# Performance work log

Measured on AMD Instinct MI355X. Metric: run time of the kernel, lower is better.

The kernel has to match this reference:

```python
import jax, jax.numpy as jnp
import numpy as np

N_NODES = 50000
N_EDGES = 600000
DIM = 128
N_LAYERS = 3
N_GRAPHS = 512
BN_EPS = 1e-5


def setup_inputs() -> dict:
    key = jax.random.key(0)
    ks = jax.random.split(key, 8)
    x = jax.random.normal(ks[0], (N_NODES, DIM), dtype=jnp.float32)
    edge_index = jax.random.randint(ks[1], (2, N_EDGES), 0, N_NODES, dtype=jnp.int32)
    batch = jnp.sort(jax.random.randint(ks[2], (N_NODES,), 0, N_GRAPHS, dtype=jnp.int32))
    W1s = jax.random.normal(ks[3], (N_LAYERS, DIM, DIM), dtype=jnp.float32) * (1.0 / np.sqrt(DIM))
    b1s = jnp.zeros((N_LAYERS, DIM), dtype=jnp.float32)
    W2s = jax.random.normal(ks[4], (N_LAYERS, DIM, DIM), dtype=jnp.float32) * (1.0 / np.sqrt(DIM))
    b2s = jnp.zeros((N_LAYERS, DIM), dtype=jnp.float32)
    gammas = jnp.ones((N_LAYERS, DIM), dtype=jnp.float32)
    betas = jnp.zeros((N_LAYERS, DIM), dtype=jnp.float32)
    return {"x": x, "edge_index": edge_index, "batch": batch,
            "W1s": W1s, "b1s": b1s, "W2s": W2s, "b2s": b2s,
            "gammas": gammas, "betas": betas}


def reference(x, edge_index, batch, W1s, b1s, W2s, b2s, gammas, betas):
    # EncoderGIN.forward: stack of GINConv (eps=0) -> ReLU -> BatchNorm1d (train mode),
    # then global_add_pool per layer and concat along feature dim.
    n_nodes = x.shape[0]
    src, dst = edge_index[0], edge_index[1]
    h = x
    pools = []
    for i in range(N_LAYERS):
        # GINConv: aggregate sum of neighbor feats at dst, add (1+0)*self
        agg = jax.ops.segment_sum(h[src], dst, num_segments=n_nodes) + h
        # MLP: Linear -> ReLU -> Linear
        h1 = jax.nn.relu(agg @ W1s[i] + b1s[i])
        h2 = h1 @ W2s[i] + b2s[i]
        # outer ReLU
        h2 = jax.nn.relu(h2)
        # BatchNorm1d, training mode (biased variance over the node dim)
        mean = jnp.mean(h2, axis=0)
        var = jnp.var(h2, axis=0)
        h = (h2 - mean) * jax.lax.rsqrt(var + BN_EPS) * gammas[i] + betas[i]
        pools.append(jax.ops.segment_sum(h, batch, num_segments=N_GRAPHS))
    return jnp.concatenate(pools, axis=1)  # [N_GRAPHS, N_LAYERS*DIM]
```

## Files before the change

### kernel.cpp

```cpp
#include <hip/hip_runtime.h>

#define N_NODES 50000
#define N_EDGES 600000
#define DIM 128
#define N_GRAPHS 512
#define N_LAYERS 3
#define OUT_STRIDE (N_LAYERS * DIM)
#define BN_EPS 1e-5f
#define N_REP 16
#define CAP 64

#define NPB 128
#define NBIN 391
#define BCAP_BIN 3072
#define PADC 16
#define EPB 4096
#define NB3 147

#define NTILES 1563
#define NPAD (NTILES * 32)
#define AGG_BLOCKS 2048

typedef __attribute__((ext_vector_type(8))) short short8;
typedef __attribute__((ext_vector_type(4))) float floatx4;

__device__ inline short f2bf(float f) {
    union { float f; unsigned u; } x{f};
    unsigned r = x.u + 0x7fffu + ((x.u >> 16) & 1u);
    return (short)(r >> 16);
}
__device__ inline float bf2f(short h) {
    union { unsigned u; float f; } x;
    x.u = ((unsigned)(unsigned short)h) << 16;
    return x.f;
}
__device__ inline void split_trunc(float f, short& hi, short& lo) {
    union { float f; unsigned u; } x{f};
    hi = (short)(x.u >> 16);
    union { unsigned u; float f; } hf;
    hf.u = x.u & 0xffff0000u;
    union { float f; unsigned u; } y{f - hf.f};
    lo = (short)(y.u >> 16);
}
__device__ inline floatx4 bf4_to_f4(uint2 w) {
    union { unsigned u; float f; } a, b, c, d;
    a.u = w.x << 16;
    b.u = w.x & 0xffff0000u;
    c.u = w.y << 16;
    d.u = w.y & 0xffff0000u;
    return floatx4{a.f, b.f, c.f, d.f};
}

__global__ __launch_bounds__(256) void prep_scatter_kernel(const int* __restrict__ src,
                                                           const int* __restrict__ dst,
                                                           int* __restrict__ binCur,
                                                           int2* __restrict__ binned,
                                                           const float* __restrict__ W1s,
                                                           const float* __restrict__ W2s,
                                                           short* __restrict__ Whi,
                                                           short* __restrict__ Wlo,
                                                           const float* __restrict__ x,
                                                           short* __restrict__ xb,
                                                           short* __restrict__ hbA,
                                                           short* __restrict__ hbB) {
    if (blockIdx.x < NB3) {
        __shared__ int hist[NBIN];
        __shared__ int basev[NBIN];
        const int t = threadIdx.x;
        for (int b = t; b < NBIN; b += 256) hist[b] = 0;
        __syncthreads();
        const int e0 = blockIdx.x * EPB;
        int sreg[16], dreg[16], rreg[16];
#pragma unroll
        for (int k = 0; k < 16; ++k) {
            int e = e0 + k * 256 + t;
            if (e < N_EDGES) {
                sreg[k] = src[e];
                dreg[k] = dst[e];
            } else {
                dreg[k] = -1;
            }
        }
#pragma unroll
        for (int k = 0; k < 16; ++k)
            if (dreg[k] >= 0) rreg[k] = atomicAdd(&hist[dreg[k] >> 7], 1);
        __syncthreads();
        for (int b = t; b < NBIN; b += 256) {
            int c = hist[b];
            basev[b] = (c > 0) ? atomicAdd(&binCur[b * PADC], c) : 0;
        }
        __syncthreads();
#pragma unroll
        for (int k = 0; k < 16; ++k)
            if (dreg[k] >= 0) {
                int b = dreg[k] >> 7;
                int pos = basev[b] + rreg[k];
                if (pos < BCAP_BIN)
                    binned[(size_t)b * BCAP_BIN + pos] = make_int2(sreg[k], dreg[k] & (NPB - 1));
            }
        return;
    }
    int i = (blockIdx.x - NB3) * 256 + threadIdx.x;
    if (i < 6 * DIM * DIM) {
        int mat = i >> 14;
        int e = i & 16383;
        int k = e >> 7, n = e & 127;
        const float* W = (mat < 3) ? (W1s + (size_t)mat * DIM * DIM)
                                   : (W2s + (size_t)(mat - 3) * DIM * DIM);
        float w = W[e];
        short hi = f2bf(w);
        short lo = f2bf(w - bf2f(hi));
        size_t o = ((size_t)mat << 14) + n * DIM + k;
        Whi[o] = hi;
        Wlo[o] = lo;
    }
    if (i < N_NODES * 32) {
        float4 v = ((const float4*)x)[i];
        unsigned lo = (unsigned short)f2bf(v.x) | ((unsigned)(unsigned short)f2bf(v.y) << 16);
        unsigned hi = (unsigned short)f2bf(v.z) | ((unsigned)(unsigned short)f2bf(v.w) << 16);
        ((uint2*)xb)[i] = make_uint2(lo, hi);
    } else if (i < (N_NODES + 1) * 32) {
        ((uint2*)xb)[i] = make_uint2(0u, 0u);
        ((uint2*)hbA)[i] = make_uint2(0u, 0u);
        ((uint2*)hbB)[i] = make_uint2(0u, 0u);
    }
}

__global__ __launch_bounds__(256) void bucket_build_kernel(const int* __restrict__ binCur,
                                                           const int2* __restrict__ binned,
                                                           int* __restrict__ deg,
                                                           int* __restrict__ esrc) {
    __shared__ int ldeg[NPB];
    __shared__ int lbuck[NPB * CAP];
    const int b = blockIdx.x;
    const int t = threadIdx.x;
    for (int i = t; i < NPB * CAP; i += 256) lbuck[i] = N_NODES;
    if (t < NPB) ldeg[t] = 0;
    __syncthreads();
    int n = binCur[b * PADC];
    if (n > BCAP_BIN) n = BCAP_BIN;
    const int2* bp = binned + (size_t)b * BCAP_BIN;
    for (int i = t; i < n; i += 256) {
        int2 e = bp[i];
        int slot = atomicAdd(&ldeg[e.y], 1);
        if (slot < CAP) lbuck[(e.y << 6) + slot] = e.x;
    }
    __syncthreads();
    const int node0 = b * NPB;
    const int nvalid = min(NPB, N_NODES - node0);
    if (t < NPB && t < nvalid) deg[node0 + t] = ldeg[t];
    const int nu4 = nvalid << 4;
    uint4* d4 = (uint4*)(esrc + ((size_t)node0 << 6));
    const uint4* s4 = (const uint4*)lbuck;
    for (int i = t; i < nu4; i += 256) d4[i] = s4[i];
}

__global__ __launch_bounds__(256) void agg_kernel(const short* __restrict__ hin,
                                                  const int* __restrict__ deg,
                                                  const int* __restrict__ esrc,
                                                  const float* __restrict__ prevrep,
                                                  const float* __restrict__ pgamma,
                                                  const float* __restrict__ pbeta,
                                                  unsigned* __restrict__ agg) {
    __shared__ float GO_s[256];
    const int tid = threadIdx.x;
    if (prevrep) {
        float s = 0.f;
#pragma unroll
        for (int r = 0; r < N_REP; ++r) s += prevrep[r * 256 + tid];
        GO_s[tid] = s;
        __syncthreads();
        if (tid < 128) {
            const float invn = 1.0f / (float)N_NODES;
            float m = GO_s[tid] * invn;
            float var = GO_s[128 + tid] * invn - m * m;
            float G = pgamma[tid] * rsqrtf(var + BN_EPS);
            GO_s[tid] = G;
            GO_s[128 + tid] = pbeta[tid] - m * G;
        }
    } else {
        GO_s[tid] = (tid < 128) ? 1.f : 0.f;
    }
    __syncthreads();

    const int hw = tid >> 5;
    const int l32 = tid & 31;
    floatx4 G4 = *(const floatx4*)&GO_s[4 * l32];
    floatx4 O4 = *(const floatx4*)&GO_s[128 + 4 * l32];
    const uint2* hb = (const uint2*)hin;

    for (int node = blockIdx.x * 8 + hw; node < NPAD; node += AGG_BLOCKS * 8) {
        floatx4 acc = {0.f, 0.f, 0.f, 0.f};
        if (node < N_NODES) {
            int dgr = deg[node];
            if (dgr > CAP) dgr = CAP;
            const uint4* ep = (const uint4*)(esrc + ((size_t)node << 6));
            uint4 q0 = ep[0], q1 = ep[1], q2 = ep[2], q3 = ep[3];
            uint2 wself = hb[(size_t)node * 32 + l32];
            uint2 wv[16];
            wv[0] = hb[(size_t)q0.x * 32 + l32];
            wv[1] = hb[(size_t)q0.y * 32 + l32];
            wv[2] = hb[(size_t)q0.z * 32 + l32];
            wv[3] = hb[(size_t)q0.w * 32 + l32];
            wv[4] = hb[(size_t)q1.x * 32 + l32];
            wv[5] = hb[(size_t)q1.y * 32 + l32];
            wv[6] = hb[(size_t)q1.z * 32 + l32];
            wv[7] = hb[(size_t)q1.w * 32 + l32];
            wv[8] = hb[(size_t)q2.x * 32 + l32];
            wv[9] = hb[(size_t)q2.y * 32 + l32];
            wv[10] = hb[(size_t)q2.z * 32 + l32];
            wv[11] = hb[(size_t)q2.w * 32 + l32];
            wv[12] = hb[(size_t)q3.x * 32 + l32];
            wv[13] = hb[(size_t)q3.y * 32 + l32];
            wv[14] = hb[(size_t)q3.z * 32 + l32];
            wv[15] = hb[(size_t)q3.w * 32 + l32];
            floatx4 t0 = (bf4_to_f4(wv[0]) + bf4_to_f4(wv[1])) + (bf4_to_f4(wv[2]) + bf4_to_f4(wv[3]));
            floatx4 t1 = (bf4_to_f4(wv[4]) + bf4_to_f4(wv[5])) + (bf4_to_f4(wv[6]) + bf4_to_f4(wv[7]));
            floatx4 t2 = (bf4_to_f4(wv[8]) + bf4_to_f4(wv[9])) + (bf4_to_f4(wv[10]) + bf4_to_f4(wv[11]));
            floatx4 t3 = (bf4_to_f4(wv[12]) + bf4_to_f4(wv[13])) + (bf4_to_f4(wv[14]) + bf4_to_f4(wv[15]));
            acc = bf4_to_f4(wself) + ((t0 + t1) + (t2 + t3));
            if (dgr > 16) {
                int b0 = node << 6;
                int jend = b0 + ((dgr + 7) & ~7);
                for (int j = b0 + 16; j < jend; j += 8) {
                    uint4 i0 = *(const uint4*)&esrc[j];
                    uint4 i1 = *(const uint4*)&esrc[j + 4];
                    uint2 w0 = hb[(size_t)i0.x * 32 + l32];
                    uint2 w1 = hb[(size_t)i0.y * 32 + l32];
                    uint2 w2 = hb[(size_t)i0.z * 32 + l32];
                    uint2 w3 = hb[(size_t)i0.w * 32 + l32];
                    uint2 w4 = hb[(size_t)i1.x * 32 + l32];
                    uint2 w5 = hb[(size_t)i1.y * 32 + l32];
                    uint2 w6 = hb[(size_t)i1.z * 32 + l32];
                    uint2 w7 = hb[(size_t)i1.w * 32 + l32];
                    acc += ((bf4_to_f4(w0) + bf4_to_f4(w1)) + (bf4_to_f4(w2) + bf4_to_f4(w3))) +
                           ((bf4_to_f4(w4) + bf4_to_f4(w5)) + (bf4_to_f4(w6) + bf4_to_f4(w7)));
                }
            }
            float dp1 = (float)(dgr + 1);
            acc = G4 * acc + dp1 * O4;
        }
        short hi[4], lo[4];
#pragma unroll
        for (int q = 0; q < 4; ++q) split_trunc(acc[q], hi[q], lo[q]);
        unsigned p0 = ((unsigned)(unsigned short)hi[0] << 16) | (unsigned short)lo[0];
        unsigned p1 = ((unsigned)(unsigned short)hi[1] << 16) | (unsigned short)lo[1];
        unsigned p2 = ((unsigned)(unsigned short)hi[2] << 16) | (unsigned short)lo[2];
        unsigned p3 = ((unsigned)(unsigned short)hi[3] << 16) | (unsigned short)lo[3];
        *(uint4*)&agg[(size_t)node * 128 + 4 * l32] = make_uint4(p0, p1, p2, p3);
    }
}

__global__ __launch_bounds__(256, 6) void mlp_kernel(
    const unsigned* __restrict__ agg,
    const short* __restrict__ W1hi, const short* __restrict__ W1lo,
    const float* __restrict__ b1,
    const short* __restrict__ W2hi, const short* __restrict__ W2lo,
    const float* __restrict__ b2,
    const int* __restrict__ batch,
    short* __restrict__ out,
    float* __restrict__ srep,
    float* __restrict__ gout,
    int layer) {
    __shared__ unsigned sbuf[4096];
    const int tid = threadIdx.x;
    const int base = blockIdx.x * 32;

    {
        const uint4* gs = (const uint4*)(agg + (size_t)base * 128);
#pragma unroll
        for (int k = 0; k < 4; ++k) {
            uint4 v = gs[k * 256 + tid];
            int idx = (k * 256 + tid) * 4;
            int row = idx >> 7, c0 = idx & 127;
            *(uint4*)&sbuf[row * 128 + (((c0 >> 2) ^ (row & 31)) << 2)] = v;
        }
    }
    __syncthreads();

    const int wave = tid >> 6;
    const int lane = tid & 63;
    const int l15 = lane & 15;
    const int quad = lane >> 4;

    floatx4 acc[2][2];
#pragma unroll
    for (int mi = 0; mi < 2; ++mi)
#pragma unroll
        for (int nl = 0; nl < 2; ++nl) acc[mi][nl] = floatx4{0.f, 0.f, 0.f, 0.f};
#pragma unroll
    for (int ks = 0; ks < 4; ++ks) {
        short8 ahi[2], alo[2], bhi[2], blo[2];
#pragma unroll
        for (int mi = 0; mi < 2; ++mi) {
            int row = mi * 16 + l15;
            int c5 = ks * 8 + quad * 2;
            unsigned w[8];
            *(uint4*)&w[0] = *(const uint4*)&sbuf[row * 128 + ((c5 ^ (row & 31)) * 4)];
            *(uint4*)&w[4] = *(const uint4*)&sbuf[row * 128 + (((c5 + 1) ^ (row & 31)) * 4)];
#pragma unroll
            for (int j = 0; j < 8; ++j) {
                ahi[mi][j] = (short)(w[j] >> 16);
                alo[mi][j] = (short)(w[j] & 0xffffu);
            }
        }
#pragma unroll
        for (int nl = 0; nl < 2; ++nl) {
            size_t p = (size_t)((wave * 2 + nl) * 16 + l15) * DIM + ks * 32 + quad * 8;
            bhi[nl] = *(const short8*)&W1hi[p];
            blo[nl] = *(const short8*)&W1lo[p];
        }
#pragma unroll
        for (int mi = 0; mi < 2; ++mi)
#pragma unroll
            for (int nl = 0; nl < 2; ++nl) {
                acc[mi][nl] = __builtin_amdgcn_mfma_f32_16x16x32_bf16(ahi[mi], bhi[nl], acc[mi][nl], 0, 0, 0);
                acc[mi][nl] = __builtin_amdgcn_mfma_f32_16x16x32_bf16(alo[mi], bhi[nl], acc[mi][nl], 0, 0, 0);
                acc[mi][nl] = __builtin_amdgcn_mfma_f32_16x16x32_bf16(ahi[mi], blo[nl], acc[mi][nl], 0, 0, 0);
            }
    }
    __syncthreads();

#pragma unroll
    for (int mi = 0; mi < 2; ++mi)
#pragma unroll
        for (int nl = 0; nl < 2; ++nl) {
            int col = (wave * 2 + nl) * 16 + l15;
            float bv = b1[col];
#pragma unroll
            for (int reg = 0; reg < 4; ++reg) {
                int row = mi * 16 + quad * 4 + reg;
                float v = fmaxf(acc[mi][nl][reg] + bv, 0.f);
                union { float f; unsigned u; } x{v};
                union { unsigned u; float f; } hf;
                hf.u = x.u & 0xffff0000u;
                union { float f; unsigned u; } y{v - hf.f};
                unsigned w = hf.u | (y.u >> 16);
                sbuf[row * 128 + ((((col >> 2) ^ (row & 31)) * 4) + (col & 3))] = w;
            }
        }
    __syncthreads();

    floatx4 acc2[2][2];
#pragma unroll
    for (int mi = 0; mi < 2; ++mi)
#pragma unroll
        for (int nl = 0; nl < 2; ++nl) acc2[mi][nl] = floatx4{0.f, 0.f, 0.f, 0.f};
#pragma unroll
    for (int ks = 0; ks < 4; ++ks) {
        short8 ahi2[2], alo2[2], bhi[2], blo[2];
#pragma unroll
        for (int mi = 0; mi < 2; ++mi) {
            int row = mi * 16 + l15;
            int c5 = ks * 8 + quad * 2;
            unsigned w[8];
            *(uint4*)&w[0] = *(const uint4*)&sbuf[row * 128 + ((c5 ^ (row & 31)) * 4)];
            *(uint4*)&w[4] = *(const uint4*)&sbuf[row * 128 + (((c5 + 1) ^ (row & 31)) * 4)];
#pragma unroll
            for (int j = 0; j < 8; ++j) {
                ahi2[mi][j] = (short)(w[j] >> 16);
                alo2[mi][j] = (short)(w[j] & 0xffffu);
            }
        }
#pragma unroll
        for (int nl = 0; nl < 2; ++nl) {
            size_t p = (size_t)((wave * 2 + nl) * 16 + l15) * DIM + ks * 32 + quad * 8;
            bhi[nl] = *(const short8*)&W2hi[p];
            blo[nl] = *(const short8*)&W2lo[p];
        }
#pragma unroll
        for (int mi = 0; mi < 2; ++mi)
#pragma unroll
            for (int nl = 0; nl < 2; ++nl) {
                acc2[mi][nl] = __builtin_amdgcn_mfma_f32_16x16x32_bf16(ahi2[mi], bhi[nl], acc2[mi][nl], 0, 0, 0);
                acc2[mi][nl] = __builtin_amdgcn_mfma_f32_16x16x32_bf16(alo2[mi], bhi[nl], acc2[mi][nl], 0, 0, 0);
                acc2[mi][nl] = __builtin_amdgcn_mfma_f32_16x16x32_bf16(ahi2[mi], blo[nl], acc2[mi][nl], 0, 0, 0);
            }
    }
    __syncthreads();

    float* pool_s = (float*)sbuf;
    float* ssum = (float*)sbuf + 384;
    float* ssq = (float*)sbuf + 512;

    const int g0 = batch[base];
    int idxr[2][4];
#pragma unroll
    for (int mi = 0; mi < 2; ++mi)
#pragma unroll
        for (int reg = 0; reg < 4; ++reg) {
            int row = base + mi * 16 + quad * 4 + reg;
            idxr[mi][reg] = (row < N_NODES) ? (batch[row] - g0) : -1;
        }

#pragma unroll
    for (int nl = 0; nl < 2; ++nl) {
        int col = (wave * 2 + nl) * 16 + l15;
        float bv = b2[col];
        float s_p = 0.f, q_p = 0.f, p0 = 0.f, p1 = 0.f, p2 = 0.f;
#pragma unroll
        for (int mi = 0; mi < 2; ++mi)
#pragma unroll
            for (int reg = 0; reg < 4; ++reg) {
                int idx = idxr[mi][reg];
                if (idx >= 0) {
                    int row = base + mi * 16 + quad * 4 + reg;
                    float v = fmaxf(acc2[mi][nl][reg] + bv, 0.f);
                    out[(size_t)row * DIM + col] = f2bf(v);
                    s_p += v;
                    q_p += v * v;
                    if (idx == 0) p0 += v;
                    else if (idx == 1) p1 += v;
                    else if (idx == 2) p2 += v;
                    else atomicAdd(&gout[(size_t)(g0 + idx) * OUT_STRIDE + layer * DIM + col], v);
                }
            }
        s_p += __shfl_xor(s_p, 16);
        s_p += __shfl_xor(s_p, 32);
        q_p += __shfl_xor(q_p, 16);
        q_p += __shfl_xor(q_p, 32);
        p0 += __shfl_xor(p0, 16);
        p0 += __shfl_xor(p0, 32);
        p1 += __shfl_xor(p1, 16);
        p1 += __shfl_xor(p1, 32);
        p2 += __shfl_xor(p2, 16);
        p2 += __shfl_xor(p2, 32);
        if (quad == 0) {
            ssum[col] = s_p;
            ssq[col] = q_p;
            pool_s[col] = p0;
            pool_s[128 + col] = p1;
            pool_s[256 + col] = p2;
        }
    }
    __syncthreads();

    float* srep_b = srep + (blockIdx.x & (N_REP - 1)) * 256;
    if (tid < 128)
        atomicAdd(&srep_b[tid], ssum[tid]);
    else
        atomicAdd(&srep_b[tid], ssq[tid - 128]);
    for (int i = tid; i < 384; i += 256) {
        int slot = i >> 7, col = i & 127;
        float pv = pool_s[slot * 128 + col];
        int g = g0 + slot;
        if (pv != 0.f && g < N_GRAPHS)
            atomicAdd(&gout[(size_t)g * OUT_STRIDE + layer * DIM + col], pv);
    }
}

__global__ __launch_bounds__(384) void finalize_kernel(const float* __restrict__ rep,
                                                       const float* __restrict__ gammas,
                                                       const float* __restrict__ betas,
                                                       const int* __restrict__ batch,
                                                       float* __restrict__ out) {
    __shared__ float cntf;
    int b = blockIdx.x;
    int t = threadIdx.x;
    if (t == 0) {
        int lo = 0, hi = N_NODES;
        while (lo < hi) {
            int m = (lo + hi) >> 1;
            if (batch[m] < b) lo = m + 1;
            else hi = m;
        }
        int lo2 = lo, hi2 = N_NODES;
        while (lo2 < hi2) {
            int m = (lo2 + hi2) >> 1;
            if (batch[m] < b + 1) lo2 = m + 1;
            else hi2 = m;
        }
        cntf = (float)(lo2 - lo);
    }
    __syncthreads();
    int l = t >> 7, c = t & 127;
    const float* rl = rep + (size_t)l * N_REP * 256;
    float s = 0.f, q = 0.f;
#pragma unroll
    for (int r = 0; r < N_REP; ++r) {
        s += rl[r * 256 + c];
        q += rl[r * 256 + 128 + c];
    }
    const float invn = 1.0f / (float)N_NODES;
    float m = s * invn;
    float var = q * invn - m * m;
    float G = gammas[l * DIM + c] * rsqrtf(var + BN_EPS);
    float OFF = betas[l * DIM + c] - m * G;
    size_t o = (size_t)b * OUT_STRIDE + t;
    out[o] = fmaf(G, out[o], cntf * OFF);
}

extern "C" void kernel_launch(void* const* d_in, const int* in_sizes, int n_in,
                              void* d_out, int out_size, void* d_ws, size_t ws_size,
                              hipStream_t stream) {
    const float* x = (const float*)d_in[0];
    const int* ei = (const int*)d_in[1];
    const int* srcp = ei;
    const int* dstp = ei + N_EDGES;
    const int* batch = (const int*)d_in[2];
    const float* W1s = (const float*)d_in[3];
    const float* b1s = (const float*)d_in[4];
    const float* W2s = (const float*)d_in[5];
    const float* b2s = (const float*)d_in[6];
    const float* gammas = (const float*)d_in[7];
    const float* betas = (const float*)d_in[8];
    float* out = (float*)d_out;

    const size_t NFR = (size_t)(N_NODES + 1) * DIM;
    short* hbufA = (short*)d_ws;
    short* hbufB = hbufA + NFR;
    short* xb = hbufB + NFR;
    short* whi = xb + NFR;
    short* wlo = whi + 6 * DIM * DIM;
    float* stats_rep = (float*)(wlo + 6 * DIM * DIM);
    int* binCur = (int*)(stats_rep + 3 * N_REP * 256);
    int* deg = binCur + NBIN * PADC;
    int* esrc = deg + N_NODES;
    unsigned* agg = (unsigned*)(esrc + (size_t)N_NODES * CAP);
    int2* binned = (int2*)hbufB;

    hipMemsetAsync(out, 0, (size_t)N_GRAPHS * OUT_STRIDE * sizeof(float), stream);
    hipMemsetAsync(stats_rep, 0,
                   (3 * N_REP * 256) * sizeof(float) + (NBIN * PADC) * sizeof(int), stream);

    prep_scatter_kernel<<<NB3 + ((N_NODES + 1) * 32 + 255) / 256, 256, 0, stream>>>(
        srcp, dstp, binCur, binned, W1s, W2s, whi, wlo, x, xb, hbufA, hbufB);
    bucket_build_kernel<<<NBIN, 256, 0, stream>>>(binCur, binned, deg, esrc);

    const short* hin = xb;
    short* hout = hbufA;
    for (int layer = 0; layer < N_LAYERS; ++layer) {
        const float* prevrep =
            (layer == 0) ? nullptr : (stats_rep + (size_t)(layer - 1) * N_REP * 256);
        agg_kernel<<<AGG_BLOCKS, 256, 0, stream>>>(
            hin, deg, esrc, prevrep, gammas + (layer - 1) * DIM, betas + (layer - 1) * DIM, agg);
        mlp_kernel<<<NTILES, 256, 0, stream>>>(
            agg, whi + ((size_t)layer << 14), wlo + ((size_t)layer << 14), b1s + layer * DIM,
            whi + ((size_t)(3 + layer) << 14), wlo + ((size_t)(3 + layer) << 14),
            b2s + layer * DIM, batch, hout, stats_rep + (size_t)layer * N_REP * 256, out, layer);
        hin = hout;
        hout = (hout == hbufA) ? hbufB : hbufA;
    }
    finalize_kernel<<<N_GRAPHS, 384, 0, stream>>>(stats_rep, gammas, betas, batch, out);
}
```

Before: 304.3 us.

## Replace MLP atomics with per-tile partials and deterministic reductions

The MLP kernel no longer issues atomicAdds for BatchNorm statistics and graph pooling. It writes per-tile partial sums to workspace instead. A small reduce kernel folds the stat partials into the replicated stats buffer, and the finalize kernel gathers the pool partials for each graph from the tiles that cover its node range. The launch-bounds occupancy hint also rises from 6 to 8 waves. This removes atomic contention and the stats memset, at the cost of an extra kernel launch per layer and more global writes and reads.

```diff
diff --git a/kernel.cpp b/kernel.cpp
--- a/kernel.cpp
+++ b/kernel.cpp
@@ -251,7 +251,7 @@
     }
 }
 
-__global__ __launch_bounds__(256, 6) void mlp_kernel(
+__global__ __launch_bounds__(256, 8) void mlp_kernel(
     const unsigned* __restrict__ agg,
     const short* __restrict__ W1hi, const short* __restrict__ W1lo,
     const float* __restrict__ b1,
@@ -259,7 +259,8 @@
     const float* __restrict__ b2,
     const int* __restrict__ batch,
     short* __restrict__ out,
-    float* __restrict__ srep,
+    float* __restrict__ stats_part,
+    float* __restrict__ pool_part,
     float* __restrict__ gout,
     int layer) {
     __shared__ unsigned sbuf[4096];
@@ -435,28 +436,30 @@
     }
     __syncthreads();
 
-    float* srep_b = srep + (blockIdx.x & (N_REP - 1)) * 256;
-    if (tid < 128)
-        atomicAdd(&srep_b[tid], ssum[tid]);
-    else
-        atomicAdd(&srep_b[tid], ssq[tid - 128]);
-    for (int i = tid; i < 384; i += 256) {
-        int slot = i >> 7, col = i & 127;
-        float pv = pool_s[slot * 128 + col];
-        int g = g0 + slot;
-        if (pv != 0.f && g < N_GRAPHS)
-            atomicAdd(&gout[(size_t)g * OUT_STRIDE + layer * DIM + col], pv);
-    }
+    stats_part[(size_t)blockIdx.x * 256 + tid] = (tid < 128) ? ssum[tid] : ssq[tid - 128];
+    for (int i = tid; i < 384; i += 256)
+        pool_part[(size_t)blockIdx.x * 384 + i] = pool_s[i];
+}
+
+__global__ __launch_bounds__(256) void reduce_stats_kernel(const float* __restrict__ sp,
+                                                           float* __restrict__ srep) {
+    const int r = blockIdx.x;
+    const int tid = threadIdx.x;
+    float s = 0.f;
+    for (int t = r; t < NTILES; t += N_REP) s += sp[(size_t)t * 256 + tid];
+    srep[r * 256 + tid] = s;
 }
 
 __global__ __launch_bounds__(384) void finalize_kernel(const float* __restrict__ rep,
+                                                       const float* __restrict__ pool_part,
                                                        const float* __restrict__ gammas,
                                                        const float* __restrict__ betas,
                                                        const int* __restrict__ batch,
                                                        float* __restrict__ out) {
     __shared__ float cntf;
-    int b = blockIdx.x;
-    int t = threadIdx.x;
+    __shared__ int stlo, sthi;
+    const int b = blockIdx.x;
+    const int t = threadIdx.x;
     if (t == 0) {
         int lo = 0, hi = N_NODES;
         while (lo < hi) {
@@ -471,9 +474,11 @@
             else hi2 = m;
         }
         cntf = (float)(lo2 - lo);
-    }
-    __syncthreads();
-    int l = t >> 7, c = t & 127;
+        stlo = lo >> 5;
+        sthi = (lo2 > lo) ? ((lo2 - 1) >> 5) : (lo >> 5) - 1;
+    }
+    __syncthreads();
+    const int l = t >> 7, c = t & 127;
     const float* rl = rep + (size_t)l * N_REP * 256;
     float s = 0.f, q = 0.f;
 #pragma unroll
@@ -486,8 +491,14 @@
     float var = q * invn - m * m;
     float G = gammas[l * DIM + c] * rsqrtf(var + BN_EPS);
     float OFF = betas[l * DIM + c] - m * G;
+    float ps = 0.f;
+    for (int tt = stlo; tt <= sthi; ++tt) {
+        int slot = b - batch[tt * 32];
+        if (slot >= 0 && slot < 3)
+            ps += pool_part[((size_t)l * NTILES + tt) * 384 + slot * 128 + c];
+    }
     size_t o = (size_t)b * OUT_STRIDE + t;
-    out[o] = fmaf(G, out[o], cntf * OFF);
+    out[o] = fmaf(G, out[o] + ps, cntf * OFF);
 }
 
 extern "C" void kernel_launch(void* const* d_in, const int* in_sizes, int n_in,
@@ -517,11 +528,12 @@
     int* deg = binCur + NBIN * PADC;
     int* esrc = deg + N_NODES;
     unsigned* agg = (unsigned*)(esrc + (size_t)N_NODES * CAP);
+    float* stats_part = (float*)(agg + (size_t)NPAD * 128);
+    float* pool_part = stats_part + (size_t)NTILES * 256;
     int2* binned = (int2*)hbufB;
 
     hipMemsetAsync(out, 0, (size_t)N_GRAPHS * OUT_STRIDE * sizeof(float), stream);
-    hipMemsetAsync(stats_rep, 0,
-                   (3 * N_REP * 256) * sizeof(float) + (NBIN * PADC) * sizeof(int), stream);
+    hipMemsetAsync(binCur, 0, (NBIN * PADC) * sizeof(int), stream);
 
     prep_scatter_kernel<<<NB3 + ((N_NODES + 1) * 32 + 255) / 256, 256, 0, stream>>>(
         srcp, dstp, binCur, binned, W1s, W2s, whi, wlo, x, xb, hbufA, hbufB);
@@ -537,9 +549,12 @@
         mlp_kernel<<<NTILES, 256, 0, stream>>>(
             agg, whi + ((size_t)layer << 14), wlo + ((size_t)layer << 14), b1s + layer * DIM,
             whi + ((size_t)(3 + layer) << 14), wlo + ((size_t)(3 + layer) << 14),
-            b2s + layer * DIM, batch, hout, stats_rep + (size_t)layer * N_REP * 256, out, layer);
+            b2s + layer * DIM, batch, hout, stats_part,
+            pool_part + (size_t)layer * NTILES * 384, out, layer);
+        reduce_stats_kernel<<<N_REP, 256, 0, stream>>>(
+            stats_part, stats_rep + (size_t)layer * N_REP * 256);
         hin = hout;
         hout = (hout == hbufA) ? hbufB : hbufA;
     }
-    finalize_kernel<<<N_GRAPHS, 384, 0, stream>>>(stats_rep, gammas, betas, batch, out);
-}
+    finalize_kernel<<<N_GRAPHS, 384, 0, stream>>>(stats_rep, pool_part, gammas, betas, batch, out);
+}
```

After: 386.4 us. 1.27x slower.
